# Optimization experiments

Hardware: AMD Instinct MI355X
Metric: run time of the kernel (lower is better)

The kernel has to match this reference:

```python
import jax, jax.numpy as jnp
import numpy as np

EMBED_DIM = 1024
NUM_HEADS = 16
HEAD_DIM = EMBED_DIM // NUM_HEADS
B, T = 2, 2048


def setup_inputs() -> dict:
    key = jax.random.key(0)
    ks = jax.random.split(key, 9)
    s = 1.0 / np.sqrt(EMBED_DIM)
    x = jax.random.normal(ks[0], (B, T, EMBED_DIM), dtype=jnp.float32)
    Wq = jax.random.uniform(ks[1], (EMBED_DIM, EMBED_DIM), jnp.float32, -s, s)
    bq = jax.random.uniform(ks[2], (EMBED_DIM,), jnp.float32, -s, s)
    Wk = jax.random.uniform(ks[3], (EMBED_DIM, EMBED_DIM), jnp.float32, -s, s)
    bk = jax.random.uniform(ks[4], (EMBED_DIM,), jnp.float32, -s, s)
    Wv = jax.random.uniform(ks[5], (EMBED_DIM, EMBED_DIM), jnp.float32, -s, s)
    bv = jax.random.uniform(ks[6], (EMBED_DIM,), jnp.float32, -s, s)
    Wo = jax.random.uniform(ks[7], (EMBED_DIM, EMBED_DIM), jnp.float32, -s, s)
    bo = jax.random.uniform(ks[8], (EMBED_DIM,), jnp.float32, -s, s)
    return {"x": x, "Wq": Wq, "bq": bq, "Wk": Wk, "bk": bk,
            "Wv": Wv, "bv": bv, "Wo": Wo, "bo": bo}


def reference(x, Wq, bq, Wk, bk, Wv, bv, Wo, bo):
    Bx, Tx, D = x.shape
    # projections (torch Linear: y = x @ W^T + b); here W stored as [in, out]
    q = (x @ Wq + bq).reshape(Bx, Tx, NUM_HEADS, HEAD_DIM).transpose(0, 2, 1, 3)
    k = (x @ Wk + bk).reshape(Bx, Tx, NUM_HEADS, HEAD_DIM).transpose(0, 2, 1, 3)
    v = (x @ Wv + bv).reshape(Bx, Tx, NUM_HEADS, HEAD_DIM).transpose(0, 2, 1, 3)
    scale = HEAD_DIM ** -0.5
    attn = jnp.einsum('bhqd,bhkd->bhqk', q, k) * scale  # [B, H, T, T]
    causal = jnp.tril(jnp.ones((Tx, Tx), dtype=bool))
    attn = jnp.where(causal[None, None], attn, -jnp.inf)
    attn = jax.nn.softmax(attn, axis=-1)
    out = jnp.einsum('bhqk,bhkd->bhqd', attn, v)  # [B, H, T, hd]
    out = out.transpose(0, 2, 1, 3).reshape(Bx, Tx, D)
    return out @ Wo + bo
```

## Files before the change

kernel.cpp:

```cpp
#include <hip/hip_runtime.h>

#define EMBED 1024
#define NHEADS 16
#define HDIM 64
#define SEQ 2048
#define BATCH 2
#define MROWS (BATCH * SEQ)

using bf16x8 = __attribute__((ext_vector_type(8))) short;
using f32x4  = __attribute__((ext_vector_type(4))) float;
using us4    = __attribute__((ext_vector_type(4))) unsigned short;

__device__ __forceinline__ unsigned short f2bf(float f) {
    unsigned int u = __builtin_bit_cast(unsigned int, f);
    u = (u + 0x7fffu + ((u >> 16) & 1u)) >> 16;
    return (unsigned short)u;
}

__device__ __forceinline__ void async16(const unsigned short* g, unsigned short* l) {
    __builtin_amdgcn_global_load_lds(
        (const __attribute__((address_space(1))) void*)g,
        (__attribute__((address_space(3))) void*)l, 16, 0, 0);
}

__global__ __launch_bounds__(256)
void cvt_x(const float* __restrict__ in, unsigned short* __restrict__ out)
{
    int i = blockIdx.x * 256 + threadIdx.x;
    float4 v = ((const float4*)in)[i];
    us4 o;
    o[0] = f2bf(v.x); o[1] = f2bf(v.y); o[2] = f2bf(v.z); o[3] = f2bf(v.w);
    ((us4*)out)[i] = o;
}

__global__ __launch_bounds__(256)
void cvt_w(const float* __restrict__ W0, const float* __restrict__ W1,
           const float* __restrict__ W2, const float* __restrict__ W3,
           unsigned short* __restrict__ T0, unsigned short* __restrict__ T1,
           unsigned short* __restrict__ T2, unsigned short* __restrict__ T3)
{
    const float* W = blockIdx.z == 0 ? W0 : blockIdx.z == 1 ? W1 :
                     blockIdx.z == 2 ? W2 : W3;
    unsigned short* T = blockIdx.z == 0 ? T0 : blockIdx.z == 1 ? T1 :
                        blockIdx.z == 2 ? T2 : T3;
    __shared__ unsigned short tile[64][72];
    const int tid = threadIdx.x;
    const int k0 = blockIdx.y << 6, n0 = blockIdx.x << 6;
    const int lr = tid >> 4, lc = (tid & 15) << 2;
#pragma unroll
    for (int it = 0; it < 4; ++it) {
        int kr = lr + it * 16;
        float4 v = *(const float4*)(W + (size_t)(k0 + kr) * EMBED + n0 + lc);
        tile[lc + 0][kr] = f2bf(v.x);
        tile[lc + 1][kr] = f2bf(v.y);
        tile[lc + 2][kr] = f2bf(v.z);
        tile[lc + 3][kr] = f2bf(v.w);
    }
    __syncthreads();
#pragma unroll
    for (int it = 0; it < 4; ++it) {
        int nr = lr + it * 16;
        us4 o = *(const us4*)(&tile[nr][lc]);
        *(us4*)(T + (size_t)(n0 + nr) * EMBED + k0 + lc) = o;
    }
}

__device__ __forceinline__ void mfma_gemm_core(
    const unsigned short* __restrict__ A, const unsigned short* __restrict__ Bt,
    int bm, int n0, unsigned short* As, unsigned short* Bs,
    int wv, int lane, f32x4 acc[4][4])
{
    const int m16 = lane & 15, quad = lane >> 4;
    const int mb = (wv >> 1) << 6;
    const int nb = (wv & 1) << 6;

    const unsigned short* ga = A  + (size_t)(bm + wv * 32 + (lane >> 3)) * EMBED + ((lane & 7) << 3);
    const unsigned short* gb = Bt + (size_t)(n0 + wv * 32 + (lane >> 3)) * EMBED + ((lane & 7) << 3);
    unsigned short* la = As + wv * 32 * 64;
    unsigned short* lb = Bs + wv * 32 * 64;

    for (int k0 = 0; k0 < EMBED; k0 += 64) {
        __syncthreads();
#pragma unroll
        for (int j = 0; j < 4; ++j) {
            async16(ga + j * 8 * EMBED, la + j * 8 * 64);
            async16(gb + j * 8 * EMBED, lb + j * 8 * 64);
        }
        ga += 64; gb += 64;
        __syncthreads();
#pragma unroll
        for (int ks = 0; ks < 2; ++ks) {
            const int ko = ks * 32 + (quad << 3);
            bf16x8 af[4], bfv[4];
#pragma unroll
            for (int i = 0; i < 4; ++i) {
                af[i]  = *(const bf16x8*)(As + (mb + i * 16 + m16) * 64 + ko);
                bfv[i] = *(const bf16x8*)(Bs + (nb + i * 16 + m16) * 64 + ko);
            }
#pragma unroll
            for (int i = 0; i < 4; ++i)
#pragma unroll
                for (int j = 0; j < 4; ++j)
                    acc[i][j] = __builtin_amdgcn_mfma_f32_16x16x32_bf16(
                        af[i], bfv[j], acc[i][j], 0, 0, 0);
        }
    }
}

__device__ __forceinline__ void mfma_gemm_core64(
    const unsigned short* __restrict__ A, const unsigned short* __restrict__ Bt,
    int bm, int n0, unsigned short* As, unsigned short* Bs,
    int wv, int lane, f32x4 acc[4][2])
{
    const int m16 = lane & 15, quad = lane >> 4;
    const int mb = (wv >> 1) << 6;
    const int nb = (wv & 1) << 5;

    const unsigned short* ga = A  + (size_t)(bm + wv * 32 + (lane >> 3)) * EMBED + ((lane & 7) << 3);
    const unsigned short* gb = Bt + (size_t)(n0 + wv * 16 + (lane >> 3)) * EMBED + ((lane & 7) << 3);
    unsigned short* la = As + wv * 32 * 64;
    unsigned short* lb = Bs + wv * 16 * 64;

    for (int k0 = 0; k0 < EMBED; k0 += 64) {
        __syncthreads();
#pragma unroll
        for (int j = 0; j < 4; ++j)
            async16(ga + j * 8 * EMBED, la + j * 8 * 64);
#pragma unroll
        for (int j = 0; j < 2; ++j)
            async16(gb + j * 8 * EMBED, lb + j * 8 * 64);
        ga += 64; gb += 64;
        __syncthreads();
#pragma unroll
        for (int ks = 0; ks < 2; ++ks) {
            const int ko = ks * 32 + (quad << 3);
            bf16x8 af[4], bfv[2];
#pragma unroll
            for (int i = 0; i < 4; ++i)
                af[i] = *(const bf16x8*)(As + (mb + i * 16 + m16) * 64 + ko);
#pragma unroll
            for (int j = 0; j < 2; ++j)
                bfv[j] = *(const bf16x8*)(Bs + (nb + j * 16 + m16) * 64 + ko);
#pragma unroll
            for (int i = 0; i < 4; ++i)
#pragma unroll
                for (int j = 0; j < 2; ++j)
                    acc[i][j] = __builtin_amdgcn_mfma_f32_16x16x32_bf16(
                        af[i], bfv[j], acc[i][j], 0, 0, 0);
        }
    }
}

__global__ __launch_bounds__(256)
void qkv_gemm(const unsigned short* __restrict__ xb,
              const unsigned short* __restrict__ Wtq,
              const unsigned short* __restrict__ Wtk,
              const unsigned short* __restrict__ Wtv,
              const float* __restrict__ bq, const float* __restrict__ bk,
              const float* __restrict__ bv,
              unsigned short* __restrict__ Qo, unsigned short* __restrict__ Ko,
              unsigned short* __restrict__ Vto)
{
    __shared__ __align__(16) unsigned short As[128 * 64];
    __shared__ __align__(16) unsigned short Bs[128 * 64];
    const int tid = threadIdx.x, wv = tid >> 6, lane = tid & 63;
    const int m16 = lane & 15, quad = lane >> 4;
    const int which = blockIdx.x >> 3;
    const int n0 = (blockIdx.x & 7) << 7;
    const int bm = blockIdx.y << 7;
    const unsigned short* Bt = which == 0 ? Wtq : which == 1 ? Wtk : Wtv;
    const float* bias = which == 0 ? bq : which == 1 ? bk : bv;

    f32x4 acc[4][4];
#pragma unroll
    for (int i = 0; i < 4; ++i)
#pragma unroll
        for (int j = 0; j < 4; ++j) acc[i][j] = (f32x4){0.f, 0.f, 0.f, 0.f};

    mfma_gemm_core(xb, Bt, bm, n0, As, Bs, wv, lane, acc);

    const int mb = (wv >> 1) << 6, nb = (wv & 1) << 6;
    const float qscale = 0.125f * 1.4426950408889634f;
#pragma unroll
    for (int i = 0; i < 4; ++i) {
        const int m0 = bm + mb + i * 16 + quad * 4;
        const int b = m0 >> 11, t0 = m0 & (SEQ - 1);
#pragma unroll
        for (int j = 0; j < 4; ++j) {
            const int n = n0 + nb + j * 16 + m16;
            const int h = n >> 6, d = n & 63;
            const float bval = bias[n];
            if (which == 2) {
                us4 v;
#pragma unroll
                for (int r = 0; r < 4; ++r) v[r] = f2bf(acc[i][j][r] + bval);
                *(us4*)(Vto + ((((size_t)(b * NHEADS + h)) << 6) + d) * SEQ + t0) = v;
            } else {
                const float sc = which == 0 ? qscale : 1.f;
                unsigned short* dst = (which == 0 ? Qo : Ko) +
                    ((((size_t)(b * NHEADS + h)) << 11) + t0) * 64 + d;
#pragma unroll
                for (int r = 0; r < 4; ++r)
                    dst[(size_t)r * 64] = f2bf((acc[i][j][r] + bval) * sc);
            }
        }
    }
}

__global__ __launch_bounds__(256)
void out_gemm(const unsigned short* __restrict__ aob,
              const unsigned short* __restrict__ Wto,
              const float* __restrict__ bo, float* __restrict__ out)
{
    __shared__ __align__(16) unsigned short As[128 * 64];
    __shared__ __align__(16) unsigned short Bs[64 * 64];
    const int tid = threadIdx.x, wv = tid >> 6, lane = tid & 63;
    const int m16 = lane & 15, quad = lane >> 4;
    const int n0 = blockIdx.x << 6;
    const int bm = blockIdx.y << 7;

    f32x4 acc[4][2];
#pragma unroll
    for (int i = 0; i < 4; ++i)
#pragma unroll
        for (int j = 0; j < 2; ++j) acc[i][j] = (f32x4){0.f, 0.f, 0.f, 0.f};

    mfma_gemm_core64(aob, Wto, bm, n0, As, Bs, wv, lane, acc);

    const int mb = (wv >> 1) << 6, nb = (wv & 1) << 5;
#pragma unroll
    for (int i = 0; i < 4; ++i) {
        const int m0 = bm + mb + i * 16 + quad * 4;
#pragma unroll
        for (int j = 0; j < 2; ++j) {
            const int n = n0 + nb + j * 16 + m16;
            const float bval = bo[n];
#pragma unroll
            for (int r = 0; r < 4; ++r)
                out[(size_t)(m0 + r) * EMBED + n] = acc[i][j][r] + bval;
        }
    }
}

__global__ __launch_bounds__(256)
void attn_mfma(const unsigned short* __restrict__ Qb,
               const unsigned short* __restrict__ Kb,
               const unsigned short* __restrict__ Vtb,
               unsigned short* __restrict__ Oout)
{
    __shared__ __align__(16) unsigned short Ks[2][64 * 72];
    __shared__ __align__(16) unsigned short Vt[2][64 * 72];
    __shared__ __align__(16) unsigned short Ps[4][16 * 72];

    const int tid  = threadIdx.x;
    const int wv   = tid >> 6;
    const int lane = tid & 63;
    const int m16  = lane & 15;
    const int quad = lane >> 4;
    const int bh   = blockIdx.y;
    const int b    = bh >> 4, h = bh & 15;

    const int srow = tid >> 2;
    const int scol = (tid & 3) << 4;

    bf16x8 rk0, rk1, rv0, rv1;
    auto load_tile = [&](int k0) {
        const unsigned short* sk = Kb + (((size_t)bh << 11) + k0 + srow) * 64 + scol;
        rk0 = *(const bf16x8*)sk;
        rk1 = *(const bf16x8*)(sk + 8);
        const unsigned short* sv = Vtb + (((size_t)bh << 6) + srow) * SEQ + k0 + scol;
        rv0 = *(const bf16x8*)sv;
        rv1 = *(const bf16x8*)(sv + 8);
    };

    for (int phase = 0; phase < 2; ++phase) {
        const int qt = phase == 0 ? (31 - (int)blockIdx.x) : (int)blockIdx.x;
        const int q0 = qt << 6;

        const size_t qoff =
            (((size_t)bh << 11) + q0 + (wv << 4) + m16) * 64 + (quad << 3);
        bf16x8 qa0 = *(const bf16x8*)(Qb + qoff);
        bf16x8 qa1 = *(const bf16x8*)(Qb + qoff + 32);

        f32x4 o[4];
#pragma unroll
        for (int dt = 0; dt < 4; ++dt) o[dt] = (f32x4){0.f, 0.f, 0.f, 0.f};
        float m_ = -1e30f, l_ = 0.f;

        load_tile(0);
        __syncthreads();

        for (int kt = 0; kt <= qt; ++kt) {
            unsigned short* Kp = Ks[kt & 1];
            unsigned short* Vp = Vt[kt & 1];
            *(bf16x8*)(Kp + srow * 72 + scol)     = rk0;
            *(bf16x8*)(Kp + srow * 72 + scol + 8) = rk1;
            *(bf16x8*)(Vp + srow * 72 + scol)     = rv0;
            *(bf16x8*)(Vp + srow * 72 + scol + 8) = rv1;
            __syncthreads();
            if (kt < qt) load_tile((kt + 1) << 6);

            const bool diag = (kt == qt);

            f32x4 s[4];
#pragma unroll
            for (int g = 0; g < 4; ++g) {
                if (diag && g > wv) {
                    s[g] = (f32x4){-1e30f, -1e30f, -1e30f, -1e30f};
                    continue;
                }
                const unsigned short* kp = Kp + (g * 16 + m16) * 72 + (quad << 3);
                bf16x8 kb0 = *(const bf16x8*)kp;
                bf16x8 kb1 = *(const bf16x8*)(kp + 32);
                s[g] = (f32x4){0.f, 0.f, 0.f, 0.f};
                s[g] = __builtin_amdgcn_mfma_f32_16x16x32_bf16(kb0, qa0, s[g], 0, 0, 0);
                s[g] = __builtin_amdgcn_mfma_f32_16x16x32_bf16(kb1, qa1, s[g], 0, 0, 0);
            }
            if (diag) {
#pragma unroll
                for (int r = 0; r < 4; ++r)
                    if (quad * 4 + r > m16) s[wv][r] = -1e30f;
            }

            float mx = s[0][0];
#pragma unroll
            for (int g = 0; g < 4; ++g)
#pragma unroll
                for (int r = 0; r < 4; ++r) mx = fmaxf(mx, s[g][r]);
            mx = fmaxf(mx, __shfl_xor(mx, 16));
            mx = fmaxf(mx, __shfl_xor(mx, 32));
            const float nm = fmaxf(m_, mx);
            const float alpha = exp2f(m_ - nm);
            float sum = 0.f;
#pragma unroll
            for (int g = 0; g < 4; ++g)
#pragma unroll
                for (int r = 0; r < 4; ++r) {
                    float p = exp2f(s[g][r] - nm);
                    s[g][r] = p;
                    sum += p;
                }
            sum += __shfl_xor(sum, 16);
            sum += __shfl_xor(sum, 32);
            l_ = l_ * alpha + sum;
            m_ = nm;

#pragma unroll
            for (int g = 0; g < 4; ++g) {
                us4 pv;
#pragma unroll
                for (int r = 0; r < 4; ++r) pv[r] = f2bf(s[g][r]);
                *(us4*)(&Ps[wv][m16 * 72 + g * 16 + quad * 4]) = pv;
            }

#pragma unroll
            for (int dt = 0; dt < 4; ++dt) o[dt] *= alpha;

            const unsigned short* pp = &Ps[wv][m16 * 72 + (quad << 3)];
            bf16x8 pa0 = *(const bf16x8*)pp;
            bf16x8 pa1 = *(const bf16x8*)(pp + 32);
            const bool skip_hi = diag && (wv < 2);
#pragma unroll
            for (int dt = 0; dt < 4; ++dt) {
                const unsigned short* vp = Vp + (dt * 16 + m16) * 72 + (quad << 3);
                bf16x8 vb0 = *(const bf16x8*)vp;
                o[dt] = __builtin_amdgcn_mfma_f32_16x16x32_bf16(vb0, pa0, o[dt], 0, 0, 0);
                if (!skip_hi) {
                    bf16x8 vb1 = *(const bf16x8*)(vp + 32);
                    o[dt] = __builtin_amdgcn_mfma_f32_16x16x32_bf16(vb1, pa1, o[dt], 0, 0, 0);
                }
            }
        }

        const float inv = 1.f / l_;
        const int t = q0 + (wv << 4) + m16;
        unsigned short* dst =
            Oout + ((size_t)((b << 11) + t) << 10) + (h << 6) + (quad << 2);
#pragma unroll
        for (int dt = 0; dt < 4; ++dt) {
            us4 w;
#pragma unroll
            for (int r = 0; r < 4; ++r) w[r] = f2bf(o[dt][r] * inv);
            *(us4*)(dst + dt * 16) = w;
        }
    }
}

extern "C" void kernel_launch(void* const* d_in, const int* in_sizes, int n_in,
                              void* d_out, int out_size, void* d_ws, size_t ws_size,
                              hipStream_t stream) {
    const float* x  = (const float*)d_in[0];
    const float* Wq = (const float*)d_in[1];
    const float* bq = (const float*)d_in[2];
    const float* Wk = (const float*)d_in[3];
    const float* bk = (const float*)d_in[4];
    const float* Wv = (const float*)d_in[5];
    const float* bv = (const float*)d_in[6];
    const float* Wo = (const float*)d_in[7];
    const float* bo = (const float*)d_in[8];
    float* out = (float*)d_out;

    const size_t HSZ = (size_t)MROWS * EMBED;
    const size_t WSZ = (size_t)EMBED * EMBED;
    unsigned short* qb  = (unsigned short*)d_ws;
    unsigned short* kb  = qb + HSZ;
    unsigned short* vtb = kb + HSZ;
    unsigned short* aob = vtb + HSZ;
    unsigned short* xb  = aob + HSZ;
    unsigned short* wtq = xb + HSZ;
    unsigned short* wtk = wtq + WSZ;
    unsigned short* wtv = wtk + WSZ;
    unsigned short* wto = wtv + WSZ;

    cvt_x<<<MROWS * EMBED / 1024, 256, 0, stream>>>(x, xb);
    cvt_w<<<dim3(16, 16, 4), 256, 0, stream>>>(Wq, Wk, Wv, Wo, wtq, wtk, wtv, wto);

    qkv_gemm<<<dim3(24, 32), 256, 0, stream>>>(xb, wtq, wtk, wtv, bq, bk, bv,
                                               qb, kb, vtb);

    attn_mfma<<<dim3(16, BATCH * NHEADS), 256, 0, stream>>>(qb, kb, vtb, aob);

    out_gemm<<<dim3(16, 32), 256, 0, stream>>>(aob, wto, bo, out);
}
```

Baseline: 223.7 us.

## Restructure causal attention to one wave per 16-query strip reading K/V from global

The attention kernel now launches 4096 single-wave blocks, each handling one 16-row query strip with heaviest strips first. The old 4-wave blocks with paired query tiles and LDS-staged K/V are gone. K and V fragments are loaded straight from global memory (relying on cache), and only the P tile goes through LDS. The max and sum reductions are rewritten as trees. This raises parallelism and removes block-wide K/V staging, but loses K/V sharing across waves, so global/L2 traffic rises.

New measurement: 392.9 us. 75.6% more time.

```diff
diff --git a/kernel.cpp b/kernel.cpp
--- a/kernel.cpp
+++ b/kernel.cpp
@@ -242,147 +242,132 @@
     }
 }
 
-__global__ __launch_bounds__(256)
+__global__ __launch_bounds__(64)
 void attn_mfma(const unsigned short* __restrict__ Qb,
                const unsigned short* __restrict__ Kb,
                const unsigned short* __restrict__ Vtb,
                unsigned short* __restrict__ Oout)
 {
-    __shared__ __align__(16) unsigned short Ks[2][64 * 72];
-    __shared__ __align__(16) unsigned short Vt[2][64 * 72];
-    __shared__ __align__(16) unsigned short Ps[4][16 * 72];
-
-    const int tid  = threadIdx.x;
-    const int wv   = tid >> 6;
-    const int lane = tid & 63;
+    __shared__ __align__(16) unsigned short Ps[16 * 72];
+
+    const int lane = threadIdx.x;
     const int m16  = lane & 15;
     const int quad = lane >> 4;
     const int bh   = blockIdx.y;
     const int b    = bh >> 4, h = bh & 15;
-
-    const int srow = tid >> 2;
-    const int scol = (tid & 3) << 4;
-
-    bf16x8 rk0, rk1, rv0, rv1;
-    auto load_tile = [&](int k0) {
-        const unsigned short* sk = Kb + (((size_t)bh << 11) + k0 + srow) * 64 + scol;
-        rk0 = *(const bf16x8*)sk;
-        rk1 = *(const bf16x8*)(sk + 8);
-        const unsigned short* sv = Vtb + (((size_t)bh << 6) + srow) * SEQ + k0 + scol;
-        rv0 = *(const bf16x8*)sv;
-        rv1 = *(const bf16x8*)(sv + 8);
-    };
-
-    for (int phase = 0; phase < 2; ++phase) {
-        const int qt = phase == 0 ? (31 - (int)blockIdx.x) : (int)blockIdx.x;
-        const int q0 = qt << 6;
-
-        const size_t qoff =
-            (((size_t)bh << 11) + q0 + (wv << 4) + m16) * 64 + (quad << 3);
-        bf16x8 qa0 = *(const bf16x8*)(Qb + qoff);
-        bf16x8 qa1 = *(const bf16x8*)(Qb + qoff + 32);
-
-        f32x4 o[4];
-#pragma unroll
-        for (int dt = 0; dt < 4; ++dt) o[dt] = (f32x4){0.f, 0.f, 0.f, 0.f};
-        float m_ = -1e30f, l_ = 0.f;
-
-        load_tile(0);
-        __syncthreads();
-
-        for (int kt = 0; kt <= qt; ++kt) {
-            unsigned short* Kp = Ks[kt & 1];
-            unsigned short* Vp = Vt[kt & 1];
-            *(bf16x8*)(Kp + srow * 72 + scol)     = rk0;
-            *(bf16x8*)(Kp + srow * 72 + scol + 8) = rk1;
-            *(bf16x8*)(Vp + srow * 72 + scol)     = rv0;
-            *(bf16x8*)(Vp + srow * 72 + scol + 8) = rv1;
-            __syncthreads();
-            if (kt < qt) load_tile((kt + 1) << 6);
-
-            const bool diag = (kt == qt);
-
-            f32x4 s[4];
-#pragma unroll
-            for (int g = 0; g < 4; ++g) {
-                if (diag && g > wv) {
-                    s[g] = (f32x4){-1e30f, -1e30f, -1e30f, -1e30f};
-                    continue;
-                }
-                const unsigned short* kp = Kp + (g * 16 + m16) * 72 + (quad << 3);
-                bf16x8 kb0 = *(const bf16x8*)kp;
-                bf16x8 kb1 = *(const bf16x8*)(kp + 32);
-                s[g] = (f32x4){0.f, 0.f, 0.f, 0.f};
-                s[g] = __builtin_amdgcn_mfma_f32_16x16x32_bf16(kb0, qa0, s[g], 0, 0, 0);
-                s[g] = __builtin_amdgcn_mfma_f32_16x16x32_bf16(kb1, qa1, s[g], 0, 0, 0);
+    const int qs   = 127 - (int)blockIdx.x;
+    const int qmod = qs & 3;
+    const int nkt  = qs >> 2;
+
+    const unsigned short* qp =
+        Qb + (((size_t)bh << 11) + (qs << 4) + m16) * 64 + (quad << 3);
+    bf16x8 qa0 = *(const bf16x8*)qp;
+    bf16x8 qa1 = *(const bf16x8*)(qp + 32);
+
+    const unsigned short* Kbase = Kb + (((size_t)bh << 11) << 6);
+    const unsigned short* Vbase = Vtb + (((size_t)bh << 6) << 11);
+
+    f32x4 o[4];
+#pragma unroll
+    for (int dt = 0; dt < 4; ++dt) o[dt] = (f32x4){0.f, 0.f, 0.f, 0.f};
+    float m_ = -1e30f, l_ = 0.f;
+
+    for (int kt = 0; kt <= nkt; ++kt) {
+        const int k0 = kt << 6;
+        const bool diag = (kt == nkt);
+
+        f32x4 s[4];
+#pragma unroll
+        for (int g = 0; g < 4; ++g) {
+            if (diag && g > qmod) {
+                s[g] = (f32x4){-1e30f, -1e30f, -1e30f, -1e30f};
+                continue;
             }
-            if (diag) {
-#pragma unroll
-                for (int r = 0; r < 4; ++r)
-                    if (quad * 4 + r > m16) s[wv][r] = -1e30f;
+            const unsigned short* kp =
+                Kbase + (size_t)(k0 + g * 16 + m16) * 64 + (quad << 3);
+            bf16x8 kb0 = *(const bf16x8*)kp;
+            bf16x8 kb1 = *(const bf16x8*)(kp + 32);
+            s[g] = (f32x4){0.f, 0.f, 0.f, 0.f};
+            s[g] = __builtin_amdgcn_mfma_f32_16x16x32_bf16(kb0, qa0, s[g], 0, 0, 0);
+            s[g] = __builtin_amdgcn_mfma_f32_16x16x32_bf16(kb1, qa1, s[g], 0, 0, 0);
+        }
+        if (diag) {
+#pragma unroll
+            for (int r = 0; r < 4; ++r)
+                if (quad * 4 + r > m16) s[qmod][r] = -1e30f;
+        }
+
+        f32x4 t01, t23, tm;
+#pragma unroll
+        for (int r = 0; r < 4; ++r) {
+            t01[r] = fmaxf(s[0][r], s[1][r]);
+            t23[r] = fmaxf(s[2][r], s[3][r]);
+            tm[r]  = fmaxf(t01[r], t23[r]);
+        }
+        float mx = fmaxf(fmaxf(tm[0], tm[1]), fmaxf(tm[2], tm[3]));
+        mx = fmaxf(mx, __shfl_xor(mx, 16));
+        mx = fmaxf(mx, __shfl_xor(mx, 32));
+        const float nm = fmaxf(m_, mx);
+        const float alpha = exp2f(m_ - nm);
+
+#pragma unroll
+        for (int g = 0; g < 4; ++g)
+#pragma unroll
+            for (int r = 0; r < 4; ++r) s[g][r] = exp2f(s[g][r] - nm);
+
+        f32x4 a01, a23, at;
+#pragma unroll
+        for (int r = 0; r < 4; ++r) {
+            a01[r] = s[0][r] + s[1][r];
+            a23[r] = s[2][r] + s[3][r];
+            at[r]  = a01[r] + a23[r];
+        }
+        float sum = (at[0] + at[1]) + (at[2] + at[3]);
+        sum += __shfl_xor(sum, 16);
+        sum += __shfl_xor(sum, 32);
+        l_ = l_ * alpha + sum;
+        m_ = nm;
+
+#pragma unroll
+        for (int g = 0; g < 4; ++g) {
+            us4 pv;
+#pragma unroll
+            for (int r = 0; r < 4; ++r) pv[r] = f2bf(s[g][r]);
+            *(us4*)(&Ps[m16 * 72 + g * 16 + quad * 4]) = pv;
+        }
+        __syncthreads();
+
+#pragma unroll
+        for (int dt = 0; dt < 4; ++dt) o[dt] *= alpha;
+
+        const unsigned short* pp = Ps + m16 * 72 + (quad << 3);
+        bf16x8 pa0 = *(const bf16x8*)pp;
+        bf16x8 pa1 = *(const bf16x8*)(pp + 32);
+        const bool skip_hi = diag && (qmod < 2);
+#pragma unroll
+        for (int dt = 0; dt < 4; ++dt) {
+            const unsigned short* vp =
+                Vbase + (size_t)(dt * 16 + m16) * SEQ + k0 + (quad << 3);
+            bf16x8 vb0 = *(const bf16x8*)vp;
+            o[dt] = __builtin_amdgcn_mfma_f32_16x16x32_bf16(vb0, pa0, o[dt], 0, 0, 0);
+            if (!skip_hi) {
+                bf16x8 vb1 = *(const bf16x8*)(vp + 32);
+                o[dt] = __builtin_amdgcn_mfma_f32_16x16x32_bf16(vb1, pa1, o[dt], 0, 0, 0);
             }
-
-            float mx = s[0][0];
-#pragma unroll
-            for (int g = 0; g < 4; ++g)
-#pragma unroll
-                for (int r = 0; r < 4; ++r) mx = fmaxf(mx, s[g][r]);
-            mx = fmaxf(mx, __shfl_xor(mx, 16));
-            mx = fmaxf(mx, __shfl_xor(mx, 32));
-            const float nm = fmaxf(m_, mx);
-            const float alpha = exp2f(m_ - nm);
-            float sum = 0.f;
-#pragma unroll
-            for (int g = 0; g < 4; ++g)
-#pragma unroll
-                for (int r = 0; r < 4; ++r) {
-                    float p = exp2f(s[g][r] - nm);
-                    s[g][r] = p;
-                    sum += p;
-                }
-            sum += __shfl_xor(sum, 16);
-            sum += __shfl_xor(sum, 32);
-            l_ = l_ * alpha + sum;
-            m_ = nm;
-
-#pragma unroll
-            for (int g = 0; g < 4; ++g) {
-                us4 pv;
-#pragma unroll
-                for (int r = 0; r < 4; ++r) pv[r] = f2bf(s[g][r]);
-                *(us4*)(&Ps[wv][m16 * 72 + g * 16 + quad * 4]) = pv;
-            }
-
-#pragma unroll
-            for (int dt = 0; dt < 4; ++dt) o[dt] *= alpha;
-
-            const unsigned short* pp = &Ps[wv][m16 * 72 + (quad << 3)];
-            bf16x8 pa0 = *(const bf16x8*)pp;
-            bf16x8 pa1 = *(const bf16x8*)(pp + 32);
-            const bool skip_hi = diag && (wv < 2);
-#pragma unroll
-            for (int dt = 0; dt < 4; ++dt) {
-                const unsigned short* vp = Vp + (dt * 16 + m16) * 72 + (quad << 3);
-                bf16x8 vb0 = *(const bf16x8*)vp;
-                o[dt] = __builtin_amdgcn_mfma_f32_16x16x32_bf16(vb0, pa0, o[dt], 0, 0, 0);
-                if (!skip_hi) {
-                    bf16x8 vb1 = *(const bf16x8*)(vp + 32);
-                    o[dt] = __builtin_amdgcn_mfma_f32_16x16x32_bf16(vb1, pa1, o[dt], 0, 0, 0);
-                }
-            }
-        }
-
-        const float inv = 1.f / l_;
-        const int t = q0 + (wv << 4) + m16;
-        unsigned short* dst =
-            Oout + ((size_t)((b << 11) + t) << 10) + (h << 6) + (quad << 2);
-#pragma unroll
-        for (int dt = 0; dt < 4; ++dt) {
-            us4 w;
-#pragma unroll
-            for (int r = 0; r < 4; ++r) w[r] = f2bf(o[dt][r] * inv);
-            *(us4*)(dst + dt * 16) = w;
-        }
+        }
+        __syncthreads();
+    }
+
+    const float inv = 1.f / l_;
+    const int t = (qs << 4) + m16;
+    unsigned short* dst =
+        Oout + ((size_t)((b << 11) + t) << 10) + (h << 6) + (quad << 2);
+#pragma unroll
+    for (int dt = 0; dt < 4; ++dt) {
+        us4 w;
+#pragma unroll
+        for (int r = 0; r < 4; ++r) w[r] = f2bf(o[dt][r] * inv);
+        *(us4*)(dst + dt * 16) = w;
     }
 }
 
@@ -418,7 +403,7 @@
     qkv_gemm<<<dim3(24, 32), 256, 0, stream>>>(xb, wtq, wtk, wtv, bq, bk, bv,
                                                qb, kb, vtb);
 
-    attn_mfma<<<dim3(16, BATCH * NHEADS), 256, 0, stream>>>(qb, kb, vtb, aob);
+    attn_mfma<<<dim3(128, BATCH * NHEADS), 64, 0, stream>>>(qb, kb, vtb, aob);
 
     out_gemm<<<dim3(16, 32), 256, 0, stream>>>(aob, wto, bo, out);
 }
```
